# Optimization experiments

Hardware: AMD Instinct MI355X
Metric: run time of the kernel (lower is better)

## Reference

```python
import jax, jax.numpy as jnp
import numpy as np


def _log_matmul(a, b):
    # log-semiring matmul: C[..., i, k] = logsumexp_j (A[..., i, j] + B[..., j, k])
    return jax.nn.logsumexp(a[..., :, :, None] + b[..., None, :, :], axis=-2)


def setup_inputs() -> dict:
    key = jax.random.key(0)
    k1, k2, k3, k4, k5 = jax.random.split(key, 5)
    B, T, K = 16, 2048, 16
    return {
        "emissions": jax.random.normal(k1, (B, T, K), dtype=jnp.float32),
        "tags": jax.random.randint(k2, (B, T), 0, K, dtype=jnp.int64),
        "transitions": jax.random.uniform(k3, (K, K), minval=-0.1, maxval=0.1, dtype=jnp.float32),
        "start_transitions": jax.random.uniform(k4, (K,), minval=-0.1, maxval=0.1, dtype=jnp.float32),
        "end_transitions": jax.random.uniform(k5, (K,), minval=-0.1, maxval=0.1, dtype=jnp.float32),
    }


def reference(emissions, tags, transitions, start_transitions, end_transitions):
    B, T, K = emissions.shape
    # --- log partition via parallel log-semiring scan ---
    # transfer[b, t, i, j] = transitions[i, j] + emissions[b, t, j]
    transfer = transitions[None, None, :, :] + emissions[:, :, None, :]  # (B, T, K, K)
    # first matrix: every row i equals start_transitions + emissions[:, 0]
    first = jnp.broadcast_to((start_transitions + emissions[:, 0])[:, None, :], (B, K, K))
    mats = jnp.concatenate([first[:, None], transfer[:, 1:]], axis=1)  # (B, T, K, K)
    cum = jax.lax.associative_scan(_log_matmul, mats, axis=1)  # cumulative log-semiring products
    final_scores = cum[:, -1, 0, :] + end_transitions  # (B, K)
    log_partition = jax.nn.logsumexp(final_scores, axis=1)  # (B,)
    # --- score of given tag sequence ---
    em_score = jnp.take_along_axis(emissions, tags[:, :, None], axis=2).squeeze(2).sum(axis=1)
    trans_score = transitions[tags[:, :-1], tags[:, 1:]].sum(axis=1)
    seq_score = (em_score + trans_score
                 + start_transitions[tags[:, 0]] + end_transitions[tags[:, -1]])
    return jnp.mean(log_partition - seq_score)
```

## Files before the change

kernel.cpp:

```cpp
#include <hip/hip_runtime.h>

#define BB 16
#define TT 2048
#define KK 16
#define NC 64
#define CL 32

__global__ __launch_bounds__(256) void crf_stage1(
    const float* __restrict__ em, const float* __restrict__ trans,
    const float* __restrict__ startT, float* __restrict__ chunkT)
{
    int blk = blockIdx.x;
    int b = blk >> 6;
    int c = blk & (NC - 1);
    int tid = threadIdx.x;
    int i = tid >> 4, k = tid & 15;

    float tcol[KK];
#pragma unroll
    for (int j = 0; j < KK; ++j) tcol[j] = trans[j * KK + k];

    const float* emB = em + ((size_t)b * TT + c * CL) * KK;

    float cur = (c == 0 ? startT[k] : trans[i * KK + k]) + emB[k];

    float e_next = emB[KK + k];
#pragma unroll 4
    for (int t = 1; t < CL; ++t) {
        float e = e_next;
        if (t + 1 < CL) e_next = emB[(t + 1) * KK + k];
        float a[KK];
#pragma unroll
        for (int j = 0; j < KK; ++j)
            a[j] = __shfl(cur, j, 16) + tcol[j];
        float m = a[0];
#pragma unroll
        for (int j = 1; j < KK; ++j) m = fmaxf(m, a[j]);
        float s = 0.f;
#pragma unroll
        for (int j = 0; j < KK; ++j) s += __expf(a[j] - m);
        cur = m + __logf(s) + e;
    }
    chunkT[(size_t)blk * 256 + k * KK + i] = cur;
}

__global__ __launch_bounds__(256) void crf_stage2(
    const float* __restrict__ chunkT, const float* __restrict__ em,
    const int* __restrict__ tags, const float* __restrict__ trans,
    const float* __restrict__ startT, const float* __restrict__ endT,
    float* __restrict__ out2T, float* __restrict__ seqp)
{
    int blk = blockIdx.x;
    int b = blk >> 3;
    int g = blk & 7;
    int tid = threadIdx.x;
    int i = tid >> 4, k = tid & 15;

    const float* base = chunkT + ((size_t)(b * NC + g * 8)) * 256;
    float cur = base[k * KK + i];

#pragma unroll
    for (int c = 1; c < 8; ++c) {
        const float* mp = base + c * 256 + k * KK;
        float mc[KK];
#pragma unroll
        for (int j = 0; j < KK; ++j) mc[j] = mp[j];
        float a[KK];
#pragma unroll
        for (int j = 0; j < KK; ++j)
            a[j] = __shfl(cur, j, 16) + mc[j];
        float m = a[0];
#pragma unroll
        for (int j = 1; j < KK; ++j) m = fmaxf(m, a[j]);
        float s = 0.f;
#pragma unroll
        for (int j = 0; j < KK; ++j) s += __expf(a[j] - m);
        cur = m + __logf(s);
    }
    out2T[(size_t)blk * 256 + k * KK + i] = cur;

    int t = g * 256 + tid;
    const int* tg = tags + (size_t)b * TT;
    int cu = tg[t];
    float part = em[((size_t)b * TT + t) * KK + cu];
    if (t + 1 < TT) part += trans[cu * KK + tg[t + 1]];
    if (t == 0) part += startT[cu];
    if (t == TT - 1) part += endT[cu];
#pragma unroll
    for (int off = 32; off; off >>= 1) part += __shfl_xor(part, off, 64);
    __shared__ float red[4];
    if ((tid & 63) == 0) red[tid >> 6] = part;
    __syncthreads();
    if (tid == 0) seqp[blk] = red[0] + red[1] + red[2] + red[3];
}

__global__ __launch_bounds__(256) void crf_stage3(
    const float* __restrict__ out2T, const float* __restrict__ seqp,
    const float* __restrict__ endT, float* __restrict__ out)
{
    int tid = threadIdx.x;
    int b = tid >> 4, k = tid & 15;

    const float* base = out2T + (size_t)b * 8 * 256;
    float v = base[k * KK + 0];
#pragma unroll
    for (int g = 1; g < 8; ++g) {
        const float* mp = base + g * 256 + k * KK;
        float mc[KK];
#pragma unroll
        for (int j = 0; j < KK; ++j) mc[j] = mp[j];
        float a[KK];
#pragma unroll
        for (int j = 0; j < KK; ++j)
            a[j] = __shfl(v, j, 16) + mc[j];
        float m = a[0];
#pragma unroll
        for (int j = 1; j < KK; ++j) m = fmaxf(m, a[j]);
        float s = 0.f;
#pragma unroll
        for (int j = 0; j < KK; ++j) s += __expf(a[j] - m);
        v = m + __logf(s);
    }
    float fv = v + endT[k];
    float m = fv;
#pragma unroll
    for (int off = 8; off; off >>= 1) m = fmaxf(m, __shfl_xor(m, off, 16));
    float s = __expf(fv - m);
#pragma unroll
    for (int off = 8; off; off >>= 1) s += __shfl_xor(s, off, 16);
    float logZ = m + __logf(s);

    float sq = (k < 8) ? seqp[b * 8 + k] : 0.f;
#pragma unroll
    for (int off = 8; off; off >>= 1) sq += __shfl_xor(sq, off, 16);

    __shared__ float red[BB];
    if (k == 0) red[b] = logZ - sq;
    __syncthreads();
    if (tid == 0) {
        float acc = 0.f;
#pragma unroll
        for (int bb = 0; bb < BB; ++bb) acc += red[bb];
        out[0] = acc * (1.f / BB);
    }
}

extern "C" void kernel_launch(void* const* d_in, const int* in_sizes, int n_in,
                              void* d_out, int out_size, void* d_ws, size_t ws_size,
                              hipStream_t stream)
{
    const float* em     = (const float*)d_in[0];
    const int*   tags   = (const int*)d_in[1];
    const float* trans  = (const float*)d_in[2];
    const float* startT = (const float*)d_in[3];
    const float* endT   = (const float*)d_in[4];
    float* out = (float*)d_out;

    float* chunkT = (float*)d_ws;
    float* out2T  = chunkT + (size_t)BB * NC * 256;
    float* seqp   = out2T + 128 * 256;

    crf_stage1<<<BB * NC, 256, 0, stream>>>(em, trans, startT, chunkT);
    crf_stage2<<<BB * 8, 256, 0, stream>>>(chunkT, em, tags, trans, startT, endT,
                                           out2T, seqp);
    crf_stage3<<<1, 256, 0, stream>>>(out2T, seqp, endT, out);
}
```

Measured before the change: 97.39 us.

## Fold final reduction into stage2 via last-block atomic counter, move seq score to stage1

Drops the separate third kernel launch. The last block of stage2 to finish, detected through an atomic counter and thread fences, now does the final combine. The sequence-score computation moves into stage1, where each chunk block has 32 threads sum its own timesteps. This saves one launch and its inter-kernel gap, at the cost of fence and atomic overhead and a serial tail on one block.

```diff
diff --git a/kernel.cpp b/kernel.cpp
--- a/kernel.cpp
+++ b/kernel.cpp
@@ -7,14 +7,18 @@
 #define CL 32
 
 __global__ __launch_bounds__(256) void crf_stage1(
-    const float* __restrict__ em, const float* __restrict__ trans,
-    const float* __restrict__ startT, float* __restrict__ chunkT)
+    const float* __restrict__ em, const int* __restrict__ tags,
+    const float* __restrict__ trans, const float* __restrict__ startT,
+    const float* __restrict__ endT, float* __restrict__ chunkT,
+    float* __restrict__ seqp, int* __restrict__ ctr)
 {
     int blk = blockIdx.x;
     int b = blk >> 6;
     int c = blk & (NC - 1);
     int tid = threadIdx.x;
     int i = tid >> 4, k = tid & 15;
+
+    if (blk == 0 && tid == 0) *ctr = 0;
 
     float tcol[KK];
 #pragma unroll
@@ -42,13 +46,25 @@
         cur = m + __logf(s) + e;
     }
     chunkT[(size_t)blk * 256 + k * KK + i] = cur;
+
+    if (tid < 32) {
+        int t = c * CL + tid;
+        const int* tg = tags + (size_t)b * TT;
+        int cu = tg[t];
+        float part = em[((size_t)b * TT + t) * KK + cu];
+        if (t + 1 < TT) part += trans[cu * KK + tg[t + 1]];
+        if (t == 0) part += startT[cu];
+        if (t == TT - 1) part += endT[cu];
+#pragma unroll
+        for (int off = 16; off; off >>= 1) part += __shfl_xor(part, off, 32);
+        if (tid == 0) seqp[blk] = part;
+    }
 }
 
 __global__ __launch_bounds__(256) void crf_stage2(
-    const float* __restrict__ chunkT, const float* __restrict__ em,
-    const int* __restrict__ tags, const float* __restrict__ trans,
-    const float* __restrict__ startT, const float* __restrict__ endT,
-    float* __restrict__ out2T, float* __restrict__ seqp)
+    const float* __restrict__ chunkT, const float* __restrict__ endT,
+    const float* __restrict__ seqp, float* __restrict__ out2T,
+    int* __restrict__ ctr, float* __restrict__ out)
 {
     int blk = blockIdx.x;
     int b = blk >> 3;
@@ -79,33 +95,23 @@
     }
     out2T[(size_t)blk * 256 + k * KK + i] = cur;
 
-    int t = g * 256 + tid;
-    const int* tg = tags + (size_t)b * TT;
-    int cu = tg[t];
-    float part = em[((size_t)b * TT + t) * KK + cu];
-    if (t + 1 < TT) part += trans[cu * KK + tg[t + 1]];
-    if (t == 0) part += startT[cu];
-    if (t == TT - 1) part += endT[cu];
+    __shared__ int lastFlag;
+    __threadfence();
+    if (tid == 0) {
+        int old = atomicAdd(ctr, 1);
+        lastFlag = (old == (BB * 8 - 1));
+    }
+    __syncthreads();
+    if (!lastFlag) return;
+    __threadfence();
+
+    int fb = tid >> 4;
+    int fk = tid & 15;
+    const float* fbase = out2T + (size_t)fb * 8 * 256;
+    float v = fbase[fk * KK + 0];
 #pragma unroll
-    for (int off = 32; off; off >>= 1) part += __shfl_xor(part, off, 64);
-    __shared__ float red[4];
-    if ((tid & 63) == 0) red[tid >> 6] = part;
-    __syncthreads();
-    if (tid == 0) seqp[blk] = red[0] + red[1] + red[2] + red[3];
-}
-
-__global__ __launch_bounds__(256) void crf_stage3(
-    const float* __restrict__ out2T, const float* __restrict__ seqp,
-    const float* __restrict__ endT, float* __restrict__ out)
-{
-    int tid = threadIdx.x;
-    int b = tid >> 4, k = tid & 15;
-
-    const float* base = out2T + (size_t)b * 8 * 256;
-    float v = base[k * KK + 0];
-#pragma unroll
-    for (int g = 1; g < 8; ++g) {
-        const float* mp = base + g * 256 + k * KK;
+    for (int g2 = 1; g2 < 8; ++g2) {
+        const float* mp = fbase + g2 * 256 + fk * KK;
         float mc[KK];
 #pragma unroll
         for (int j = 0; j < KK; ++j) mc[j] = mp[j];
@@ -121,7 +127,7 @@
         for (int j = 0; j < KK; ++j) s += __expf(a[j] - m);
         v = m + __logf(s);
     }
-    float fv = v + endT[k];
+    float fv = v + endT[fk];
     float m = fv;
 #pragma unroll
     for (int off = 8; off; off >>= 1) m = fmaxf(m, __shfl_xor(m, off, 16));
@@ -130,12 +136,13 @@
     for (int off = 8; off; off >>= 1) s += __shfl_xor(s, off, 16);
     float logZ = m + __logf(s);
 
-    float sq = (k < 8) ? seqp[b * 8 + k] : 0.f;
+    float sq = seqp[fb * NC + fk] + seqp[fb * NC + fk + 16]
+             + seqp[fb * NC + fk + 32] + seqp[fb * NC + fk + 48];
 #pragma unroll
     for (int off = 8; off; off >>= 1) sq += __shfl_xor(sq, off, 16);
 
     __shared__ float red[BB];
-    if (k == 0) red[b] = logZ - sq;
+    if (fk == 0) red[fb] = logZ - sq;
     __syncthreads();
     if (tid == 0) {
         float acc = 0.f;
@@ -159,9 +166,9 @@
     float* chunkT = (float*)d_ws;
     float* out2T  = chunkT + (size_t)BB * NC * 256;
     float* seqp   = out2T + 128 * 256;
+    int*   ctr    = (int*)(seqp + BB * NC);
 
-    crf_stage1<<<BB * NC, 256, 0, stream>>>(em, trans, startT, chunkT);
-    crf_stage2<<<BB * 8, 256, 0, stream>>>(chunkT, em, tags, trans, startT, endT,
-                                           out2T, seqp);
-    crf_stage3<<<1, 256, 0, stream>>>(out2T, seqp, endT, out);
+    crf_stage1<<<BB * NC, 256, 0, stream>>>(em, tags, trans, startT, endT,
+                                            chunkT, seqp, ctr);
+    crf_stage2<<<BB * 8, 256, 0, stream>>>(chunkT, endT, seqp, out2T, ctr, out);
 }
```

Measured after the change: 110.7 us. +13.6%, slower.
